# Kernel tuning notes

Hardware: AMD Instinct MI355X
Metric: run time of the kernel (lower is better)

Reference implementation:

```python
import jax, jax.numpy as jnp
import numpy as np

B, N, PAST = 2, 1024, 1024
DIM, HEADS, DH = 2048, 16, 128
INNER = HEADS * DH
LN_EPS = 1e-5
ROPE_THETA = 10000.0


def setup_inputs() -> dict:
    key = jax.random.key(0)
    k0, k1, k2, k3, k4 = jax.random.split(key, 5)
    x = jax.random.normal(k0, (B, N, DIM), dtype=jnp.float32)
    past_k = jax.random.normal(k1, (B, HEADS, PAST, DH), dtype=jnp.float32)
    past_v = jax.random.normal(k2, (B, HEADS, PAST, DH), dtype=jnp.float32)
    # causal mask with KV-cache offset: query i sits at global pos PAST+i,
    # mask (True = blocked) keys at positions j > PAST+i
    kv = PAST + N
    q_pos = PAST + jnp.arange(N)
    k_pos = jnp.arange(kv)
    mask = jnp.broadcast_to((k_pos[None, :] > q_pos[:, None])[None, None], (B, 1, N, kv))
    w_qkv = jax.random.normal(k3, (DIM, 3 * INNER), dtype=jnp.float32) * (DIM ** -0.5)
    w_out = jax.random.normal(k4, (INNER, DIM), dtype=jnp.float32) * (INNER ** -0.5)
    ln_g = jnp.ones((DIM,), dtype=jnp.float32)
    ln_b = jnp.zeros((DIM,), dtype=jnp.float32)
    return {"x": x, "past_k": past_k, "past_v": past_v, "mask": mask,
            "w_qkv": w_qkv, "w_out": w_out, "ln_g": ln_g, "ln_b": ln_b}


def _layernorm(x, g, b):
    mu = jnp.mean(x, axis=-1, keepdims=True)
    var = jnp.mean((x - mu) ** 2, axis=-1, keepdims=True)
    return (x - mu) * jax.lax.rsqrt(var + LN_EPS) * g + b


def _rope(t, pos):
    # interleaved rotary (lucidrains rotary-embedding-torch convention)
    inv_freq = 1.0 / (ROPE_THETA ** (jnp.arange(0, DH, 2, dtype=jnp.float32) / DH))
    freqs = pos.astype(jnp.float32)[:, None] * inv_freq[None, :]   # [n, DH/2]
    freqs = jnp.repeat(freqs, 2, axis=-1)                          # [n, DH]
    cos = jnp.cos(freqs).astype(t.dtype)
    sin = jnp.sin(freqs).astype(t.dtype)
    t2 = t.reshape(*t.shape[:-1], DH // 2, 2)
    rot = jnp.stack((-t2[..., 1], t2[..., 0]), axis=-1).reshape(t.shape)
    return t * cos + rot * sin


def reference(x, past_k, past_v, mask, w_qkv, w_out, ln_g, ln_b):
    b, n, _ = x.shape
    xn = _layernorm(x, ln_g, ln_b)
    qkv = xn @ w_qkv                                               # [b, n, 3*INNER]
    q, k, v = jnp.split(qkv, 3, axis=-1)
    to_heads = lambda t: t.reshape(b, n, HEADS, DH).transpose(0, 2, 1, 3)  # b h n d
    q, k, v = to_heads(q), to_heads(k), to_heads(v)
    k = jnp.concatenate((past_k, k), axis=2)                       # [b, h, kv, d]
    v = jnp.concatenate((past_v, v), axis=2)
    kv_len = k.shape[2]
    q = _rope(q, jnp.arange(n) + (kv_len - n))
    k = _rope(k, jnp.arange(kv_len))
    scale = DH ** -0.5
    dots = jnp.einsum('bhnd,bhmd->bhnm', q, k) * scale             # [b, h, n, kv]
    dots = jnp.where(mask, -jnp.inf, dots)
    attn = jax.nn.softmax(dots, axis=-1)
    out = jnp.einsum('bhnm,bhmd->bhnd', attn, v)                   # [b, h, n, d]
    out = out.transpose(0, 2, 1, 3).reshape(b, n, INNER)
    return out @ w_out, k, v
```

## Files before the change

kernel.cpp:

```cpp
#include <hip/hip_runtime.h>
#include <hip/hip_bf16.h>
#include <math.h>

#define BB    2
#define NN    1024
#define PAST  1024
#define KVL   2048
#define DIM   2048
#define HEADS 16
#define DH    128
#define INNER 2048
#define NQKV  6144
#define TOK   2048
#define LN_EPS 1e-5f

typedef __attribute__((ext_vector_type(8)))  short    short8;
typedef __attribute__((ext_vector_type(4)))  float    f32x4;
typedef __attribute__((ext_vector_type(16))) float    f32x16;
typedef __attribute__((ext_vector_type(8)))  unsigned short us8;
typedef __attribute__((ext_vector_type(4)))  unsigned short us4;
typedef unsigned short us;

__device__ __forceinline__ float bfbits2f(us u) {
    return __uint_as_float(((unsigned int)u) << 16);
}
__device__ __forceinline__ us f2bfb(float f) {
    union { __hip_bfloat16 h; us u; } cv;
    cv.h = __float2bfloat16(f);
    return cv.u;
}
__device__ __forceinline__ unsigned pkbf(float a, float b) {
    return (unsigned)f2bfb(a) | ((unsigned)f2bfb(b) << 16);
}
__device__ __forceinline__ us8 pack8u(float4 a, float4 b) {
    us8 r;
    r[0] = f2bfb(a.x); r[1] = f2bfb(a.y); r[2] = f2bfb(a.z); r[3] = f2bfb(a.w);
    r[4] = f2bfb(b.x); r[5] = f2bfb(b.y); r[6] = f2bfb(b.z); r[7] = f2bfb(b.w);
    return r;
}

__device__ __forceinline__ void gload_lds16(const void* gsrc, void* ldst) {
    __builtin_amdgcn_global_load_lds(
        (const __attribute__((address_space(1))) void*)gsrc,
        (__attribute__((address_space(3))) void*)ldst, 16, 0, 0);
}

__global__ __launch_bounds__(256) void transp_kernel(
    const float* __restrict__ src, us* __restrict__ dst, int R, int C)
{
    const int c0 = blockIdx.x * 64;
    const int r0 = blockIdx.y * 64;
    const int tid = threadIdx.x;

    __shared__ us T[64][68];

    #pragma unroll
    for (int e = 0; e < 4; e++) {
        int idx = tid + e * 256;
        int jr  = idx >> 4;
        int c4  = (idx & 15) * 4;
        float4 v = *reinterpret_cast<const float4*>(
            src + (size_t)(r0 + jr) * C + c0 + c4);
        us4 w;
        w[0] = f2bfb(v.x); w[1] = f2bfb(v.y); w[2] = f2bfb(v.z); w[3] = f2bfb(v.w);
        *reinterpret_cast<us4*>(&T[jr][c4]) = w;
    }
    __syncthreads();

    #pragma unroll
    for (int e = 0; e < 4; e++) {
        int idx = tid + e * 256;
        int d   = idx >> 4;
        int k4  = (idx & 15) * 4;
        us4 w;
        w[0] = T[k4 + 0][d];
        w[1] = T[k4 + 1][d];
        w[2] = T[k4 + 2][d];
        w[3] = T[k4 + 3][d];
        *reinterpret_cast<us4*>(dst + (size_t)(c0 + d) * R + r0 + k4) = w;
    }
}

__global__ __launch_bounds__(256) void ln_kernel(
    const float* __restrict__ x, const float* __restrict__ g,
    const float* __restrict__ b, us* __restrict__ xn)
{
    const int t   = blockIdx.x;
    const int tid = threadIdx.x;
    const size_t base = (size_t)t * DIM;

    float4 p0 = reinterpret_cast<const float4*>(x + base)[tid * 2 + 0];
    float4 p1 = reinterpret_cast<const float4*>(x + base)[tid * 2 + 1];
    float v[8] = {p0.x, p0.y, p0.z, p0.w, p1.x, p1.y, p1.z, p1.w};

    float s1 = 0.f, s2 = 0.f;
    #pragma unroll
    for (int i = 0; i < 8; i++) { s1 += v[i]; s2 += v[i] * v[i]; }

    #pragma unroll
    for (int off = 32; off; off >>= 1) {
        s1 += __shfl_xor(s1, off);
        s2 += __shfl_xor(s2, off);
    }
    __shared__ float red1[4], red2[4];
    if ((tid & 63) == 0) { red1[tid >> 6] = s1; red2[tid >> 6] = s2; }
    __syncthreads();
    float S1 = red1[0] + red1[1] + red1[2] + red1[3];
    float S2 = red2[0] + red2[1] + red2[2] + red2[3];
    const float inv = 1.0f / (float)DIM;
    float mu  = S1 * inv;
    float var = S2 * inv - mu * mu;
    float rstd = rsqrtf(var + LN_EPS);

    const int d0 = tid * 8;
    float4 oa, ob;
    oa.x = (v[0] - mu) * rstd * g[d0 + 0] + b[d0 + 0];
    oa.y = (v[1] - mu) * rstd * g[d0 + 1] + b[d0 + 1];
    oa.z = (v[2] - mu) * rstd * g[d0 + 2] + b[d0 + 2];
    oa.w = (v[3] - mu) * rstd * g[d0 + 3] + b[d0 + 3];
    ob.x = (v[4] - mu) * rstd * g[d0 + 4] + b[d0 + 4];
    ob.y = (v[5] - mu) * rstd * g[d0 + 5] + b[d0 + 5];
    ob.z = (v[6] - mu) * rstd * g[d0 + 6] + b[d0 + 6];
    ob.w = (v[7] - mu) * rstd * g[d0 + 7] + b[d0 + 7];

    *reinterpret_cast<us8*>(xn + base + d0) = pack8u(oa, ob);
}

template<bool OUT_BF16>
__global__ __launch_bounds__(256) void gemm_bt_kernel(
    const us* __restrict__ A, const us* __restrict__ Bt,
    void* __restrict__ Cout, int M, int N, int K)
{
    __shared__ us As[3][128 * 32];
    __shared__ us Bs[3][128 * 32];

    const int tid  = threadIdx.x;
    const int wave = tid >> 6, lane = tid & 63;
    const int quad = lane >> 4, l16 = lane & 15;
    const int wm = wave & 1, wn = wave >> 1;
    const int m0 = blockIdx.y * 128, n0 = blockIdx.x * 128;

    f32x4 acc[4][4];
    #pragma unroll
    for (int i = 0; i < 4; i++)
        #pragma unroll
        for (int j = 0; j < 4; j++)
            #pragma unroll
            for (int r = 0; r < 4; r++) acc[i][j][r] = 0.f;

    auto stage = [&](int k0, int buf) {
        #pragma unroll
        for (int e = 0; e < 2; e++) {
            int phys = (e * 256 + tid) * 16;
            int lr   = phys >> 7;
            int offp = (phys & 127) ^ ((lr & 7) << 4);
            int m    = 2 * lr + (offp >> 6);
            int kb   = offp & 63;
            gload_lds16((const char*)(A + (size_t)(m0 + m) * K + k0) + kb,
                        (char*)&As[buf][0] + phys);
            gload_lds16((const char*)(Bt + (size_t)(n0 + m) * K + k0) + kb,
                        (char*)&Bs[buf][0] + phys);
        }
    };

    const int ns = K >> 5;
    stage(0, 0);
    stage(32, 1);
    __builtin_amdgcn_sched_barrier(0);
    asm volatile("s_waitcnt vmcnt(4)" ::: "memory");
    __builtin_amdgcn_s_barrier();
    __builtin_amdgcn_sched_barrier(0);

    int cur = 0;
    for (int ks = 0; ks < ns; ks++) {
        if (ks + 2 < ns) stage((ks + 2) * 32, (ks + 2) % 3);

        short8 af[4], bf[4];
        #pragma unroll
        for (int mi = 0; mi < 4; mi++) {
            int mrow = wm * 64 + mi * 16 + l16;
            int lr   = mrow >> 1;
            int off  = ((mrow & 1) * 64 + quad * 16) ^ ((lr & 7) << 4);
            af[mi] = *reinterpret_cast<const short8*>(
                (const char*)&As[cur][0] + lr * 128 + off);
        }
        #pragma unroll
        for (int ni = 0; ni < 4; ni++) {
            int nrow = wn * 64 + ni * 16 + l16;
            int lr   = nrow >> 1;
            int off  = ((nrow & 1) * 64 + quad * 16) ^ ((lr & 7) << 4);
            bf[ni] = *reinterpret_cast<const short8*>(
                (const char*)&Bs[cur][0] + lr * 128 + off);
        }

        __builtin_amdgcn_s_setprio(1);
        #pragma unroll
        for (int mi = 0; mi < 4; mi++)
            #pragma unroll
            for (int ni = 0; ni < 4; ni++)
                acc[mi][ni] = __builtin_amdgcn_mfma_f32_16x16x32_bf16(
                    af[mi], bf[ni], acc[mi][ni], 0, 0, 0);
        __builtin_amdgcn_s_setprio(0);

        __builtin_amdgcn_sched_barrier(0);
        if (ks + 2 < ns) asm volatile("s_waitcnt vmcnt(4)" ::: "memory");
        else             asm volatile("s_waitcnt vmcnt(0)" ::: "memory");
        __builtin_amdgcn_s_barrier();
        __builtin_amdgcn_sched_barrier(0);
        cur = (cur == 2) ? 0 : cur + 1;
    }

    #pragma unroll
    for (int mi = 0; mi < 4; mi++) {
        #pragma unroll
        for (int r = 0; r < 4; r++) {
            size_t row = (size_t)(m0 + wm * 64 + mi * 16 + quad * 4 + r);
            #pragma unroll
            for (int ni = 0; ni < 4; ni++) {
                size_t col = n0 + wn * 64 + ni * 16 + l16;
                if (OUT_BF16)
                    ((us*)Cout)[row * N + col] = f2bfb(acc[mi][ni][r]);
                else
                    ((float*)Cout)[row * N + col] = acc[mi][ni][r];
            }
        }
    }
}

__global__ __launch_bounds__(256) void rope_kernel(
    const float* __restrict__ past_k, const float* __restrict__ past_v,
    us* __restrict__ qkv, float* __restrict__ out_k, float* __restrict__ out_v,
    us* __restrict__ Kbf)
{
    const int tid  = threadIdx.x;
    const int pid  = blockIdx.x * 4 + (tid >> 6);
    const int lane = tid & 63;

    const int b   = pid / (HEADS * KVL);
    const int rem = pid - b * (HEADS * KVL);
    const int h   = rem / KVL;
    const int pos = rem - h * KVL;

    const float invf = exp2f((float)lane * (-13.287712379549449f / 64.0f));
    float sn, cs;
    sincosf((float)pos * invf, &sn, &cs);

    const size_t obase = ((size_t)(b * HEADS + h) * KVL + pos) * DH + 2 * lane;

    float k0, k1;
    if (pos < PAST) {
        const size_t pbase = ((size_t)(b * HEADS + h) * PAST + pos) * DH + 2 * lane;
        k0 = past_k[pbase];
        k1 = past_k[pbase + 1];
    } else {
        const int t = b * NN + (pos - PAST);
        const us* qp = qkv + (size_t)t * NQKV + INNER + h * DH + 2 * lane;
        k0 = bfbits2f(qp[0]); k1 = bfbits2f(qp[1]);
    }
    float kr0 = k0 * cs - k1 * sn;
    float kr1 = k1 * cs + k0 * sn;
    out_k[obase]     = kr0;
    out_k[obase + 1] = kr1;
    Kbf[obase]       = f2bfb(kr0);
    Kbf[obase + 1]   = f2bfb(kr1);

    if (pos < PAST) {
        const size_t pbase = ((size_t)(b * HEADS + h) * PAST + pos) * DH + 2 * lane;
        out_v[obase]     = past_v[pbase];
        out_v[obase + 1] = past_v[pbase + 1];
    } else {
        const int t = b * NN + (pos - PAST);
        const us* vp = qkv + (size_t)t * NQKV + 2 * INNER + h * DH + 2 * lane;
        out_v[obase]     = bfbits2f(vp[0]);
        out_v[obase + 1] = bfbits2f(vp[1]);
    }

    if (pos >= PAST) {
        const int t = b * NN + (pos - PAST);
        us* qq = qkv + (size_t)t * NQKV + h * DH + 2 * lane;
        float q0 = bfbits2f(qq[0]), q1 = bfbits2f(qq[1]);
        qq[0] = f2bfb(q0 * cs - q1 * sn);
        qq[1] = f2bfb(q1 * cs + q0 * sn);
    }
}

__global__ __launch_bounds__(256) void vtrans_kernel(
    const float* __restrict__ Vc, us* __restrict__ Vtg)
{
    const int jb = blockIdx.x;
    const int db = blockIdx.y;
    const int bh = blockIdx.z;
    const int tid = threadIdx.x;

    __shared__ us T[64][68];

    const float* src = Vc + ((size_t)bh * KVL + jb * 64) * DH + db * 64;
    #pragma unroll
    for (int e = 0; e < 4; e++) {
        int idx = tid + e * 256;
        int jr  = idx >> 4;
        int c4  = (idx & 15) * 4;
        float4 v = *reinterpret_cast<const float4*>(src + (size_t)jr * DH + c4);
        us4 w;
        w[0] = f2bfb(v.x); w[1] = f2bfb(v.y); w[2] = f2bfb(v.z); w[3] = f2bfb(v.w);
        *reinterpret_cast<us4*>(&T[jr][c4]) = w;
    }
    __syncthreads();

    us* dst = Vtg + ((size_t)bh * DH + db * 64) * KVL + jb * 64;
    #pragma unroll
    for (int e = 0; e < 4; e++) {
        int idx = tid + e * 256;
        int d   = idx >> 4;
        int k4  = (idx & 15) * 4;
        us4 w;
        w[0] = T[k4 + 0][d];
        w[1] = T[k4 + 1][d];
        w[2] = T[k4 + 2][d];
        w[3] = T[k4 + 3][d];
        *reinterpret_cast<us4*>(dst + (size_t)d * KVL + k4) = w;
    }
}

__global__ __launch_bounds__(512) void attn_mfma_kernel(
    const us* __restrict__ qkv,
    const us* __restrict__ Kbf,
    const us* __restrict__ Vtg,
    us* __restrict__ Ao)
{
    const int tid  = threadIdx.x;
    const int wave = tid >> 6;
    const int lane = tid & 63;
    const int l32  = lane & 31;
    const int g    = lane >> 5;
    const int wv   = wave & 3;
    const int mypar= wave >> 2;

    const int flat = blockIdx.x;
    const int s    = flat >> 3;
    const int grp  = (flat & 7) + 8 * (s & 3);
    const int p    = s >> 2;
    const int h    = grp & 15;
    const int b    = grp >> 4;
    const int qtile = (wv < 2) ? p : (15 - p);
    const int qsub  = (wv & 1) * 32;
    const int mynch = 17 + qtile;
    const int nch   = 32 - p;
    const int nit   = (nch + 1) >> 1;

    __shared__ us Ks[2][2 * 64 * 128];
    __shared__ us Vt[2][2 * 64 * 128];

    short8 qf[8];
    {
        const int qrow = qtile * 64 + qsub + l32;
        const us* qp = qkv + (size_t)(b * NN + qrow) * NQKV + h * DH;
        #pragma unroll
        for (int ks = 0; ks < 8; ks++)
            qf[ks] = *reinterpret_cast<const short8*>(qp + ks * 16 + g * 8);
    }

    f32x16 Oacc[4];
    #pragma unroll
    for (int dt = 0; dt < 4; dt++)
        #pragma unroll
        for (int r = 0; r < 16; r++) Oacc[dt][r] = 0.f;
    float m_run  = -INFINITY;
    float l_part = 0.f;

    const us* kptr = Kbf + (size_t)(b * HEADS + h) * KVL * DH;
    const us* vtb  = Vtg + (size_t)(b * HEADS + h) * DH * KVL;
    const float scale = 0.08838834764831845f;
    const float THRU  = 90.50966799f;
    const int qgmin = PAST + qtile * 64 + qsub;
    const int qg    = qgmin + l32;

    auto stage = [&](int it2, int buf) {
        #pragma unroll
        for (int e = 0; e < 4; e++) {
            int phys = (e * 512 + tid) * 16;
            int par  = phys >> 14;
            int pc   = phys & 16383;
            int row  = pc >> 8;
            int col  = (pc & 255) ^ ((row & 15) << 4);
            int j0   = (2 * it2 + par) * 64;
            gload_lds16((const char*)(kptr + (size_t)(j0 + row) * DH) + col,
                        (char*)&Ks[buf][0] + phys);
        }
        #pragma unroll
        for (int e = 0; e < 4; e++) {
            int phys = (e * 512 + tid) * 16;
            int par  = phys >> 14;
            int pc   = phys & 16383;
            int row  = pc >> 8;
            int offp = (pc & 255) ^ ((row & 15) << 4);
            int d    = row + 64 * (offp >> 7);
            int cb   = offp & 127;
            int j0   = (2 * it2 + par) * 64;
            gload_lds16((const char*)(vtb + (size_t)d * KVL) + j0 * 2 + cb,
                        (char*)&Vt[buf][0] + phys);
        }
    };

    stage(0, 0);
    asm volatile("s_waitcnt vmcnt(0)" ::: "memory");
    __builtin_amdgcn_s_barrier();
    __builtin_amdgcn_sched_barrier(0);

    int cur = 0;
    for (int it = 0; it < nit; it++) {
        if (it + 1 < nit) stage(it + 1, cur ^ 1);

        const int c = 2 * it + mypar;
        if (c < mynch) {
            const int j0 = c * 64;
            const char* kbase = (const char*)&Ks[cur][0] + mypar * 16384;
            const char* vbase = (const char*)&Vt[cur][0] + mypar * 16384;

            f32x16 S[2];
            #pragma unroll
            for (int t = 0; t < 2; t++)
                #pragma unroll
                for (int r = 0; r < 16; r++) S[t][r] = 0.f;

            __builtin_amdgcn_s_setprio(1);
            #pragma unroll
            for (int ks = 0; ks < 8; ks++) {
                #pragma unroll
                for (int t = 0; t < 2; t++) {
                    int row  = t * 32 + l32;
                    int colb = ks * 32 + g * 16;
                    const char* kp = kbase +
                                     row * 256 + (colb ^ ((row & 15) << 4));
                    short8 kb = *reinterpret_cast<const short8*>(kp);
                    S[t] = __builtin_amdgcn_mfma_f32_32x32x16_bf16(
                        kb, qf[ks], S[t], 0, 0, 0);
                }
            }
            __builtin_amdgcn_s_setprio(0);

            if (j0 + 63 > qgmin) {
                const int rel = qg - j0;
                #pragma unroll
                for (int t = 0; t < 2; t++)
                    #pragma unroll
                    for (int r = 0; r < 16; r++) {
                        int kvo = t * 32 + (r & 3) + 8 * (r >> 2) + 4 * g;
                        S[t][r] = (kvo <= rel) ? S[t][r] : -INFINITY;
                    }
            }
            float mx = -INFINITY;
            #pragma unroll
            for (int t = 0; t < 2; t++)
                #pragma unroll
                for (int r = 0; r < 16; r++) mx = fmaxf(mx, S[t][r]);
            mx = fmaxf(mx, __shfl_xor(mx, 32));

            float alpha = 1.f;
            if (__any(mx > m_run + THRU)) {
                float nm = fmaxf(m_run, mx);
                alpha = __expf((m_run - nm) * scale);
                m_run = nm;
                #pragma unroll
                for (int r = 0; r < 16; r++) {
                    float ar = __shfl(alpha, (r & 3) + 8 * (r >> 2) + 4 * g);
                    Oacc[0][r] *= ar; Oacc[1][r] *= ar;
                    Oacc[2][r] *= ar; Oacc[3][r] *= ar;
                }
            }

            const float nmk = -m_run * scale;
            float rs = 0.f;
            #pragma unroll
            for (int t = 0; t < 2; t++)
                #pragma unroll
                for (int r = 0; r < 16; r++) {
                    float pv = __expf(fmaf(S[t][r], scale, nmk));
                    S[t][r] = pv;
                    rs += pv;
                }
            l_part = l_part * alpha + rs;

            short8 paf[4];
            #pragma unroll
            for (int t = 0; t < 2; t++)
                #pragma unroll
                for (int u = 0; u < 2; u++) {
                    unsigned cA = pkbf(S[t][8*u + 0], S[t][8*u + 1]);
                    unsigned cB = pkbf(S[t][8*u + 2], S[t][8*u + 3]);
                    unsigned dA = pkbf(S[t][8*u + 4], S[t][8*u + 5]);
                    unsigned dB = pkbf(S[t][8*u + 6], S[t][8*u + 7]);
                    asm volatile("v_permlane32_swap_b32 %0, %1"
                                 : "+v"(cA), "+v"(dA));
                    asm volatile("v_permlane32_swap_b32 %0, %1"
                                 : "+v"(cB), "+v"(dB));
                    union { unsigned u4[4]; short8 s8; } fb;
                    fb.u4[0] = cA; fb.u4[1] = cB; fb.u4[2] = dA; fb.u4[3] = dB;
                    paf[t * 2 + u] = fb.s8;
                }

            __builtin_amdgcn_s_setprio(1);
            #pragma unroll
            for (int ks = 0; ks < 4; ks++) {
                #pragma unroll
                for (int dt = 0; dt < 4; dt++) {
                    int d    = dt * 32 + l32;
                    int lr   = d & 63;
                    int off  = (((d >> 6) << 7) + ks * 32 + g * 16)
                               ^ ((lr & 15) << 4);
                    const char* vp = vbase + lr * 256 + off;
                    short8 vb = *reinterpret_cast<const short8*>(vp);
                    Oacc[dt] = __builtin_amdgcn_mfma_f32_32x32x16_bf16(
                        paf[ks], vb, Oacc[dt], 0, 0, 0);
                }
            }
            __builtin_amdgcn_s_setprio(0);
        }

        __builtin_amdgcn_sched_barrier(0);
        asm volatile("s_waitcnt vmcnt(0)" ::: "memory");
        __builtin_amdgcn_s_barrier();
        __builtin_amdgcn_sched_barrier(0);
        cur ^= 1;
    }

    l_part += __shfl_xor(l_part, 32);

    float* scr = (float*)&Ks[0][0];
    float* Sm  = scr;
    float* Sl  = scr + 256;
    float* SO  = scr + 512;

    if (mypar == 1) {
        Sm[wv * 64 + lane] = m_run;
        Sl[wv * 64 + lane] = l_part;
        float* ob = SO + wv * 4096 + lane;
        #pragma unroll
        for (int dt = 0; dt < 4; dt++)
            #pragma unroll
            for (int r = 0; r < 16; r++)
                ob[(dt * 16 + r) * 64] = Oacc[dt][r];
    }
    __syncthreads();
    if (mypar == 0) {
        float m1 = Sm[wv * 64 + lane];
        float l1 = Sl[wv * 64 + lane];
        float M  = fmaxf(m_run, m1);
        float f0 = __expf((m_run - M) * scale);
        float f1 = __expf((m1 - M) * scale);
        float linv = 1.f / (l_part * f0 + l1 * f1);

        const float* ob = SO + wv * 4096 + lane;
        #pragma unroll
        for (int r = 0; r < 16; r++) {
            int qr = (r & 3) + 8 * (r >> 2) + 4 * g;
            float ivr = __shfl(linv, qr);
            float f0r = __shfl(f0, qr);
            float f1r = __shfl(f1, qr);
            int qrow = qtile * 64 + qsub + qr;
            us* dst = Ao + (size_t)(b * NN + qrow) * INNER + h * DH + l32;
            #pragma unroll
            for (int dt = 0; dt < 4; dt++) {
                float o1 = ob[(dt * 16 + r) * 64];
                dst[dt * 32] = f2bfb((Oacc[dt][r] * f0r + o1 * f1r) * ivr);
            }
        }
    }
}

extern "C" void kernel_launch(void* const* d_in, const int* in_sizes, int n_in,
                              void* d_out, int out_size, void* d_ws, size_t ws_size,
                              hipStream_t stream)
{
    const float* x      = (const float*)d_in[0];
    const float* past_k = (const float*)d_in[1];
    const float* past_v = (const float*)d_in[2];
    const float* w_qkv  = (const float*)d_in[4];
    const float* w_out  = (const float*)d_in[5];
    const float* ln_g   = (const float*)d_in[6];
    const float* ln_b   = (const float*)d_in[7];

    float* out   = (float*)d_out;
    float* out_k = out   + (size_t)BB * NN * DIM;
    float* out_v = out_k + (size_t)BB * HEADS * KVL * DH;

    us* xn   = (us*)d_ws;
    us* qkv  = xn  + (size_t)TOK * DIM;
    us* Wqt  = qkv + (size_t)TOK * NQKV;
    us* Wot  = Wqt + (size_t)NQKV * DIM;
    us* Vtg  = Wot + (size_t)DIM * INNER;
    us* attn = xn;
    us* Kbf  = Wqt;

    transp_kernel<<<dim3(NQKV / 64, DIM / 64), 256, 0, stream>>>(
        w_qkv, Wqt, DIM, NQKV);
    transp_kernel<<<dim3(DIM / 64, INNER / 64), 256, 0, stream>>>(
        w_out, Wot, INNER, DIM);

    ln_kernel<<<TOK, 256, 0, stream>>>(x, ln_g, ln_b, xn);

    gemm_bt_kernel<true><<<dim3(NQKV / 128, TOK / 128), 256, 0, stream>>>(
        xn, Wqt, (void*)qkv, TOK, NQKV, DIM);

    rope_kernel<<<(BB * HEADS * KVL) / 4, 256, 0, stream>>>(
        past_k, past_v, qkv, out_k, out_v, Kbf);

    vtrans_kernel<<<dim3(KVL / 64, DH / 64, BB * HEADS), 256, 0, stream>>>(
        out_v, Vtg);

    attn_mfma_kernel<<<256, 512, 0, stream>>>(
        qkv, Kbf, Vtg, attn);

    gemm_bt_kernel<false><<<dim3(DIM / 128, TOK / 128), 256, 0, stream>>>(
        attn, Wot, (void*)out, TOK, DIM, INNER);
}
```

Before: 362.9 us.

## Replace LDS double-buffered K/V staging with direct global loads in attention

Removes the shared-memory staging pipeline (async global-to-LDS copies, swizzle, and per-iteration barriers) and has each wave read its K and V fragments straight from global memory or cache. Each wave now loops independently over its own chunks, with no block-wide synchronisation. Shared memory shrinks to just the merge scratch, and launch bounds request two blocks per CU for more occupancy. The cost is uncoalesced-ish per-lane 16-byte global reads with no LDS reuse between waves sharing the same K/V tiles, plus exposed load latency before the MFMAs.

Result: slower. 423.7 us (+16.7%).

```diff
diff --git a/kernel.cpp b/kernel.cpp
--- a/kernel.cpp
+++ b/kernel.cpp
@@ -322,7 +322,7 @@
     }
 }
 
-__global__ __launch_bounds__(512) void attn_mfma_kernel(
+__global__ __launch_bounds__(512, 2) void attn_mfma_kernel(
     const us* __restrict__ qkv,
     const us* __restrict__ Kbf,
     const us* __restrict__ Vtg,
@@ -345,11 +345,10 @@
     const int qtile = (wv < 2) ? p : (15 - p);
     const int qsub  = (wv & 1) * 32;
     const int mynch = 17 + qtile;
-    const int nch   = 32 - p;
-    const int nit   = (nch + 1) >> 1;
-
-    __shared__ us Ks[2][2 * 64 * 128];
-    __shared__ us Vt[2][2 * 64 * 128];
+
+    __shared__ float Sm[4][64];
+    __shared__ float Sl[4][64];
+    __shared__ float SO[4][64 * 64];
 
     short8 qf[8];
     {
@@ -375,166 +374,111 @@
     const int qgmin = PAST + qtile * 64 + qsub;
     const int qg    = qgmin + l32;
 
-    auto stage = [&](int it2, int buf) {
-        #pragma unroll
-        for (int e = 0; e < 4; e++) {
-            int phys = (e * 512 + tid) * 16;
-            int par  = phys >> 14;
-            int pc   = phys & 16383;
-            int row  = pc >> 8;
-            int col  = (pc & 255) ^ ((row & 15) << 4);
-            int j0   = (2 * it2 + par) * 64;
-            gload_lds16((const char*)(kptr + (size_t)(j0 + row) * DH) + col,
-                        (char*)&Ks[buf][0] + phys);
-        }
-        #pragma unroll
-        for (int e = 0; e < 4; e++) {
-            int phys = (e * 512 + tid) * 16;
-            int par  = phys >> 14;
-            int pc   = phys & 16383;
-            int row  = pc >> 8;
-            int offp = (pc & 255) ^ ((row & 15) << 4);
-            int d    = row + 64 * (offp >> 7);
-            int cb   = offp & 127;
-            int j0   = (2 * it2 + par) * 64;
-            gload_lds16((const char*)(vtb + (size_t)d * KVL) + j0 * 2 + cb,
-                        (char*)&Vt[buf][0] + phys);
-        }
-    };
-
-    stage(0, 0);
-    asm volatile("s_waitcnt vmcnt(0)" ::: "memory");
-    __builtin_amdgcn_s_barrier();
-    __builtin_amdgcn_sched_barrier(0);
-
-    int cur = 0;
-    for (int it = 0; it < nit; it++) {
-        if (it + 1 < nit) stage(it + 1, cur ^ 1);
-
-        const int c = 2 * it + mypar;
-        if (c < mynch) {
-            const int j0 = c * 64;
-            const char* kbase = (const char*)&Ks[cur][0] + mypar * 16384;
-            const char* vbase = (const char*)&Vt[cur][0] + mypar * 16384;
-
-            f32x16 S[2];
-            #pragma unroll
-            for (int t = 0; t < 2; t++)
-                #pragma unroll
-                for (int r = 0; r < 16; r++) S[t][r] = 0.f;
-
-            __builtin_amdgcn_s_setprio(1);
-            #pragma unroll
-            for (int ks = 0; ks < 8; ks++) {
-                #pragma unroll
-                for (int t = 0; t < 2; t++) {
-                    int row  = t * 32 + l32;
-                    int colb = ks * 32 + g * 16;
-                    const char* kp = kbase +
-                                     row * 256 + (colb ^ ((row & 15) << 4));
-                    short8 kb = *reinterpret_cast<const short8*>(kp);
-                    S[t] = __builtin_amdgcn_mfma_f32_32x32x16_bf16(
-                        kb, qf[ks], S[t], 0, 0, 0);
-                }
-            }
-            __builtin_amdgcn_s_setprio(0);
-
-            if (j0 + 63 > qgmin) {
-                const int rel = qg - j0;
-                #pragma unroll
-                for (int t = 0; t < 2; t++)
-                    #pragma unroll
-                    for (int r = 0; r < 16; r++) {
-                        int kvo = t * 32 + (r & 3) + 8 * (r >> 2) + 4 * g;
-                        S[t][r] = (kvo <= rel) ? S[t][r] : -INFINITY;
-                    }
-            }
-            float mx = -INFINITY;
-            #pragma unroll
-            for (int t = 0; t < 2; t++)
-                #pragma unroll
-                for (int r = 0; r < 16; r++) mx = fmaxf(mx, S[t][r]);
-            mx = fmaxf(mx, __shfl_xor(mx, 32));
-
-            float alpha = 1.f;
-            if (__any(mx > m_run + THRU)) {
-                float nm = fmaxf(m_run, mx);
-                alpha = __expf((m_run - nm) * scale);
-                m_run = nm;
-                #pragma unroll
-                for (int r = 0; r < 16; r++) {
-                    float ar = __shfl(alpha, (r & 3) + 8 * (r >> 2) + 4 * g);
-                    Oacc[0][r] *= ar; Oacc[1][r] *= ar;
-                    Oacc[2][r] *= ar; Oacc[3][r] *= ar;
-                }
-            }
-
-            const float nmk = -m_run * scale;
-            float rs = 0.f;
+    const us* kfl = kptr + (size_t)l32 * DH + g * 8;
+    const us* vfl = vtb  + (size_t)l32 * KVL + g * 8;
+
+    for (int c = mypar; c < mynch; c += 2) {
+        const int j0 = c * 64;
+
+        f32x16 S[2];
+        #pragma unroll
+        for (int t = 0; t < 2; t++)
+            #pragma unroll
+            for (int r = 0; r < 16; r++) S[t][r] = 0.f;
+
+        __builtin_amdgcn_s_setprio(1);
+        #pragma unroll
+        for (int ks = 0; ks < 8; ks++) {
+            #pragma unroll
+            for (int t = 0; t < 2; t++) {
+                short8 kb = *reinterpret_cast<const short8*>(
+                    kfl + (size_t)(j0 + t * 32) * DH + ks * 16);
+                S[t] = __builtin_amdgcn_mfma_f32_32x32x16_bf16(
+                    kb, qf[ks], S[t], 0, 0, 0);
+            }
+        }
+        __builtin_amdgcn_s_setprio(0);
+
+        if (j0 + 63 > qgmin) {
+            const int rel = qg - j0;
             #pragma unroll
             for (int t = 0; t < 2; t++)
                 #pragma unroll
                 for (int r = 0; r < 16; r++) {
-                    float pv = __expf(fmaf(S[t][r], scale, nmk));
-                    S[t][r] = pv;
-                    rs += pv;
+                    int kvo = t * 32 + (r & 3) + 8 * (r >> 2) + 4 * g;
+                    S[t][r] = (kvo <= rel) ? S[t][r] : -INFINITY;
                 }
-            l_part = l_part * alpha + rs;
-
-            short8 paf[4];
-            #pragma unroll
-            for (int t = 0; t < 2; t++)
-                #pragma unroll
-                for (int u = 0; u < 2; u++) {
-                    unsigned cA = pkbf(S[t][8*u + 0], S[t][8*u + 1]);
-                    unsigned cB = pkbf(S[t][8*u + 2], S[t][8*u + 3]);
-                    unsigned dA = pkbf(S[t][8*u + 4], S[t][8*u + 5]);
-                    unsigned dB = pkbf(S[t][8*u + 6], S[t][8*u + 7]);
-                    asm volatile("v_permlane32_swap_b32 %0, %1"
-                                 : "+v"(cA), "+v"(dA));
-                    asm volatile("v_permlane32_swap_b32 %0, %1"
-                                 : "+v"(cB), "+v"(dB));
-                    union { unsigned u4[4]; short8 s8; } fb;
-                    fb.u4[0] = cA; fb.u4[1] = cB; fb.u4[2] = dA; fb.u4[3] = dB;
-                    paf[t * 2 + u] = fb.s8;
-                }
-
-            __builtin_amdgcn_s_setprio(1);
-            #pragma unroll
-            for (int ks = 0; ks < 4; ks++) {
-                #pragma unroll
-                for (int dt = 0; dt < 4; dt++) {
-                    int d    = dt * 32 + l32;
-                    int lr   = d & 63;
-                    int off  = (((d >> 6) << 7) + ks * 32 + g * 16)
-                               ^ ((lr & 15) << 4);
-                    const char* vp = vbase + lr * 256 + off;
-                    short8 vb = *reinterpret_cast<const short8*>(vp);
-                    Oacc[dt] = __builtin_amdgcn_mfma_f32_32x32x16_bf16(
-                        paf[ks], vb, Oacc[dt], 0, 0, 0);
-                }
-            }
-            __builtin_amdgcn_s_setprio(0);
-        }
-
-        __builtin_amdgcn_sched_barrier(0);
-        asm volatile("s_waitcnt vmcnt(0)" ::: "memory");
-        __builtin_amdgcn_s_barrier();
-        __builtin_amdgcn_sched_barrier(0);
-        cur ^= 1;
+        }
+        float mx = -INFINITY;
+        #pragma unroll
+        for (int t = 0; t < 2; t++)
+            #pragma unroll
+            for (int r = 0; r < 16; r++) mx = fmaxf(mx, S[t][r]);
+        mx = fmaxf(mx, __shfl_xor(mx, 32));
+
+        float alpha = 1.f;
+        if (__any(mx > m_run + THRU)) {
+            float nm = fmaxf(m_run, mx);
+            alpha = __expf((m_run - nm) * scale);
+            m_run = nm;
+            #pragma unroll
+            for (int r = 0; r < 16; r++) {
+                float ar = __shfl(alpha, (r & 3) + 8 * (r >> 2) + 4 * g);
+                Oacc[0][r] *= ar; Oacc[1][r] *= ar;
+                Oacc[2][r] *= ar; Oacc[3][r] *= ar;
+            }
+        }
+
+        const float nmk = -m_run * scale;
+        float rs = 0.f;
+        #pragma unroll
+        for (int t = 0; t < 2; t++)
+            #pragma unroll
+            for (int r = 0; r < 16; r++) {
+                float pv = __expf(fmaf(S[t][r], scale, nmk));
+                S[t][r] = pv;
+                rs += pv;
+            }
+        l_part = l_part * alpha + rs;
+
+        short8 paf[4];
+        #pragma unroll
+        for (int t = 0; t < 2; t++)
+            #pragma unroll
+            for (int u = 0; u < 2; u++) {
+                unsigned cA = pkbf(S[t][8*u + 0], S[t][8*u + 1]);
+                unsigned cB = pkbf(S[t][8*u + 2], S[t][8*u + 3]);
+                unsigned dA = pkbf(S[t][8*u + 4], S[t][8*u + 5]);
+                unsigned dB = pkbf(S[t][8*u + 6], S[t][8*u + 7]);
+                asm volatile("v_permlane32_swap_b32 %0, %1"
+                             : "+v"(cA), "+v"(dA));
+                asm volatile("v_permlane32_swap_b32 %0, %1"
+                             : "+v"(cB), "+v"(dB));
+                union { unsigned u4[4]; short8 s8; } fb;
+                fb.u4[0] = cA; fb.u4[1] = cB; fb.u4[2] = dA; fb.u4[3] = dB;
+                paf[t * 2 + u] = fb.s8;
+            }
+
+        __builtin_amdgcn_s_setprio(1);
+        #pragma unroll
+        for (int ks = 0; ks < 4; ks++) {
+            #pragma unroll
+            for (int dt = 0; dt < 4; dt++) {
+                short8 vb = *reinterpret_cast<const short8*>(
+                    vfl + (size_t)(dt * 32) * KVL + j0 + ks * 16);
+                Oacc[dt] = __builtin_amdgcn_mfma_f32_32x32x16_bf16(
+                    paf[ks], vb, Oacc[dt], 0, 0, 0);
+            }
+        }
+        __builtin_amdgcn_s_setprio(0);
     }
 
     l_part += __shfl_xor(l_part, 32);
 
-    float* scr = (float*)&Ks[0][0];
-    float* Sm  = scr;
-    float* Sl  = scr + 256;
-    float* SO  = scr + 512;
-
     if (mypar == 1) {
-        Sm[wv * 64 + lane] = m_run;
-        Sl[wv * 64 + lane] = l_part;
-        float* ob = SO + wv * 4096 + lane;
+        Sm[wv][lane] = m_run;
+        Sl[wv][lane] = l_part;
+        float* ob = &SO[wv][lane];
         #pragma unroll
         for (int dt = 0; dt < 4; dt++)
             #pragma unroll
@@ -543,14 +487,14 @@
     }
     __syncthreads();
     if (mypar == 0) {
-        float m1 = Sm[wv * 64 + lane];
-        float l1 = Sl[wv * 64 + lane];
+        float m1 = Sm[wv][lane];
+        float l1 = Sl[wv][lane];
         float M  = fmaxf(m_run, m1);
         float f0 = __expf((m_run - M) * scale);
         float f1 = __expf((m1 - M) * scale);
         float linv = 1.f / (l_part * f0 + l1 * f1);
 
-        const float* ob = SO + wv * 4096 + lane;
+        const float* ob = &SO[wv][lane];
         #pragma unroll
         for (int r = 0; r < 16; r++) {
             int qr = (r & 3) + 8 * (r >> 2) + 4 * g;
```
